# Kernel optimization log

Measured on AMD Instinct MI355X. Metric: run time of the kernel, lower is better.

## Reference

```python
import jax, jax.numpy as jnp
import numpy as np

K_HOPS = 2  # SGConv K = nlayers


def setup_inputs() -> dict:
    key = jax.random.key(0)
    k1, k2, k3 = jax.random.split(key, 3)
    N, E, F, C = 100000, 1600000, 128, 40
    x = jax.random.normal(k1, (N, F), dtype=jnp.float32)
    edge_index = jax.random.randint(k2, (2, E), 0, N, dtype=jnp.int64)
    W = jax.random.normal(k3, (C, F), dtype=jnp.float32) * (1.0 / np.sqrt(F))
    b = jnp.zeros((C,), dtype=jnp.float32)
    return {"x": x, "edge_index": edge_index, "W": W, "b": b}


def reference(x, edge_index, W, b):
    # SGConv: K hops of GCN-normalized propagation (with self-loops), then Linear.
    N = x.shape[0]
    loop = jnp.arange(N, dtype=edge_index.dtype)
    src = jnp.concatenate([edge_index[0], loop])  # message source
    dst = jnp.concatenate([edge_index[1], loop])  # aggregation target
    w = jnp.ones(src.shape[0], dtype=x.dtype)     # edge_weight=None -> 1, self-loop fill=1
    deg = jax.ops.segment_sum(w, dst, num_segments=N)  # in-degree incl. self-loop (>=1)
    dinv = jax.lax.rsqrt(deg)
    norm = dinv[src] * w * dinv[dst]              # D^{-1/2} A D^{-1/2}
    h = x
    for _ in range(K_HOPS):
        h = jax.ops.segment_sum(norm[:, None] * h[src], dst, num_segments=N)
    return h @ W.T + b
```

## Files before the change

kernel.cpp:

```cpp
#include <hip/hip_runtime.h>
#include <hip/hip_fp16.h>
#include <cstdint>

#define CDIM 40
#define FDIM 128
#define BIN_SHIFT 8
#define BIN_SZ (1 << BIN_SHIFT)
#define CHUNK 4096
#define STAGE_CAP 8192

typedef _Float16 f16x8 __attribute__((ext_vector_type(8)));
typedef float f32x4 __attribute__((ext_vector_type(4)));

static __device__ __forceinline__ long long load_idx(const void* p, int is64, long long i) {
    if (is64) return ((const long long*)p)[i];
    return (long long)((const int*)p)[i];
}

static __device__ __forceinline__ unsigned packh2(float a, float b) {
    __half2 h;
    h.x = __float2half(a);
    h.y = __float2half(b);
    return *(unsigned*)&h;
}

static __device__ __forceinline__ void addv4(float* acc, uint4 v) {
    const __half2* h = (const __half2*)&v;
    float2 f0 = __half22float2(h[0]);
    float2 f1 = __half22float2(h[1]);
    float2 f2 = __half22float2(h[2]);
    float2 f3 = __half22float2(h[3]);
    acc[0] += f0.x; acc[1] += f0.y; acc[2] += f1.x; acc[3] += f1.y;
    acc[4] += f2.x; acc[5] += f2.y; acc[6] += f3.x; acc[7] += f3.y;
}

static __device__ __forceinline__ f16x8 cvt8(float4 a, float4 b) {
    f16x8 r;
    r[0] = (_Float16)a.x; r[1] = (_Float16)a.y; r[2] = (_Float16)a.z; r[3] = (_Float16)a.w;
    r[4] = (_Float16)b.x; r[5] = (_Float16)b.y; r[6] = (_Float16)b.z; r[7] = (_Float16)b.w;
    return r;
}

__global__ void k_init(int* cursor, int nb, int capRec,
                       __half* gA0, __half* gB0, __half* gA1, __half* gB1, int N) {
    int i = blockIdx.x * blockDim.x + threadIdx.x;
    if (i < nb) cursor[i] = i * capRec;
    if (i < 40) {
        if (i < 16)      ((unsigned*)(gA0 + (size_t)N * 32))[i] = 0u;
        else if (i < 20) ((unsigned*)(gB0 + (size_t)N * 8))[i - 16] = 0u;
        else if (i < 36) ((unsigned*)(gA1 + (size_t)N * 32))[i - 20] = 0u;
        else             ((unsigned*)(gB1 + (size_t)N * 8))[i - 36] = 0u;
    }
}

__global__ __launch_bounds__(256) void kA3(const void* ei, long long E,
                                           int nb, int* __restrict__ cursor,
                                           unsigned* __restrict__ binned) {
    __shared__ unsigned lval[CHUNK];
    __shared__ unsigned short lbin[CHUNK];
    __shared__ int lcnt[512];
    __shared__ int lbase[512];
    __shared__ int lflag;
    int tid = threadIdx.x;
    if (tid == 0) lflag = 1;
    for (int i = tid; i < nb; i += 256) lcnt[i] = 0;
    __syncthreads();
    {
        const unsigned* w = (const unsigned*)ei;
        int nscan = (int)((2 * E < 4096) ? (2 * E) : 4096);
        for (int k = 1 + 2 * tid; k < nscan; k += 512)
            if (w[k] != 0u) lflag = 0;
    }
    __syncthreads();
    int is64 = lflag;
    long long base = (long long)blockIdx.x * CHUNK;
    int nk = (int)min((long long)CHUNK, E - base);
    for (int k = tid; k < nk; k += 256) {
        long long e = base + k;
        int s = (int)load_idx(ei, is64, e);
        int d = (int)load_idx(ei, is64, E + e);
        int bin = d >> BIN_SHIFT;
        lval[k] = (unsigned)s | ((unsigned)(d & (BIN_SZ - 1)) << 17);
        lbin[k] = (unsigned short)bin;
        atomicAdd(&lcnt[bin], 1);
    }
    __syncthreads();
    for (int i = tid; i < nb; i += 256) {
        int c = lcnt[i];
        lbase[i] = c ? atomicAdd(&cursor[i], c) : 0;
        lcnt[i] = 0;
    }
    __syncthreads();
    for (int k = tid; k < nk; k += 256) {
        int bin = lbin[k];
        int loc = atomicAdd(&lcnt[bin], 1);
        binned[lbase[bin] + loc] = lval[k];
    }
}

__global__ __launch_bounds__(256) void kBG(const unsigned* __restrict__ binned,
                                           const int* __restrict__ cursor,
                                           int capRec, int capC,
                                           int2* __restrict__ meta,
                                           int* __restrict__ cursorG,
                                           int* __restrict__ csr,
                                           const float* __restrict__ x,
                                           const float* __restrict__ W,
                                           __half* __restrict__ gA,
                                           __half* __restrict__ gB, int N) {
    __shared__ int lcnt[BIN_SZ];
    __shared__ int lsum[4];
    __shared__ int dh[64];
    __shared__ float dinvL[BIN_SZ];
    __shared__ int stage[STAGE_CAP];
    int b = blockIdx.x, tid = threadIdx.x;
    const int wid = tid >> 6;
    const int lane = tid & 63;
    int node0 = b << BIN_SHIFT;
    int nn = min(BIN_SZ, N - node0);
    int recBase = b * capRec;
    int csrBase = b * capC;
    int nedges = cursor[b] - recBase;

    lcnt[tid] = 0;
    if (tid < 64) dh[tid] = 0;
    __syncthreads();
    for (int t = tid; t < nedges; t += 256)
        atomicAdd(&lcnt[(binned[recBase + t] >> 17) & (BIN_SZ - 1)], 1);
    __syncthreads();
    int myc = lcnt[tid];
    int psz = (myc + 3) & ~3;
    int incl = psz;
#pragma unroll
    for (int off = 1; off < 64; off <<= 1) {
        int up = __shfl_up(incl, off, 64);
        if (lane >= off) incl += up;
    }
    if (lane == 63) lsum[wid] = incl;
    if (tid < nn) {
        dinvL[tid] = rsqrtf(1.0f + (float)myc);
        atomicAdd(&dh[min(myc, 63)], 1);
    } else {
        dinvL[tid] = 0.0f;
    }
    __syncthreads();
    int woff = 0;
#pragma unroll
    for (int w = 0; w < 4; ++w) woff += (w < wid) ? lsum[w] : 0;
    int ex = woff + incl - psz;
    int total = lsum[0] + lsum[1] + lsum[2] + lsum[3];
    if (wid == 0) {
        int dv = dh[lane];
        int di = dv;
#pragma unroll
        for (int off = 1; off < 64; off <<= 1) {
            int up = __shfl_up(di, off, 64);
            if (lane >= off) di += up;
        }
        dh[lane] = di - dv;
    }
    __syncthreads();
    if (tid < nn) {
        int pos = atomicAdd(&dh[min(myc, 63)], 1);
        int2 mi;
        mi.x = csrBase + ex;
        mi.y = (node0 + tid) | (myc << 17);
        meta[node0 + pos] = mi;
    }
    __syncthreads();
    lcnt[tid] = ex;
    __syncthreads();
    if (total <= STAGE_CAP) {
        for (int t = tid; t < total; t += 256) stage[t] = N;
        __syncthreads();
        for (int t = tid; t < nedges; t += 256) {
            unsigned v = binned[recBase + t];
            int src = (int)(v & 0x1FFFFu);
            int dl  = (int)((v >> 17) & (BIN_SZ - 1));
            int p = atomicAdd(&lcnt[dl], 1);
            stage[p] = src;
        }
        __syncthreads();
        const int4* sp = (const int4*)stage;
        int4* cp = (int4*)(csr + csrBase);
        for (int t = tid; t < (total >> 2); t += 256) cp[t] = sp[t];
    } else {
        if (tid < nn) cursorG[node0 + tid] = csrBase + ex;
        __syncthreads();
        for (int t = tid; t < nedges; t += 256) {
            unsigned v = binned[recBase + t];
            int src = (int)(v & 0x1FFFFu);
            int dl  = (int)((v >> 17) & (BIN_SZ - 1));
            int p = atomicAdd(&cursorG[node0 + dl], 1);
            csr[p] = src;
        }
        if (tid < nn)
            for (int k = myc; k < psz; ++k) csr[csrBase + ex + k] = N;
    }
    __syncthreads();

    const int m = lane & 15;
    const int quad = lane >> 4;
    f16x8 bfrag[3][4];
#pragma unroll
    for (int t = 0; t < 3; ++t) {
        int c = t * 16 + m;
#pragma unroll
        for (int q = 0; q < 4; ++q) {
            if (c < CDIM) {
                const float* wp = W + (size_t)c * FDIM + q * 32 + quad * 8;
                float4 w0 = *(const float4*)wp;
                float4 w1 = *(const float4*)(wp + 4);
                bfrag[t][q] = cvt8(w0, w1);
            } else {
                f16x8 z = {0, 0, 0, 0, 0, 0, 0, 0};
                bfrag[t][q] = z;
            }
        }
    }
#pragma unroll
    for (int i = 0; i < 4; ++i) {
        int lnode = wid * 64 + i * 16;
        int nodebase = node0 + lnode;
        if (nodebase >= N) break;
        const float* xp = x + (size_t)(nodebase + m) * FDIM + quad * 8;
        f16x8 afrag[4];
#pragma unroll
        for (int q = 0; q < 4; ++q) {
            float4 x0 = *(const float4*)(xp + q * 32);
            float4 x1 = *(const float4*)(xp + q * 32 + 4);
            afrag[q] = cvt8(x0, x1);
        }
        f32x4 acc0 = {0, 0, 0, 0}, acc1 = {0, 0, 0, 0}, acc2 = {0, 0, 0, 0};
#pragma unroll
        for (int q = 0; q < 4; ++q) {
            acc0 = __builtin_amdgcn_mfma_f32_16x16x32_f16(afrag[q], bfrag[0][q], acc0, 0, 0, 0);
            acc1 = __builtin_amdgcn_mfma_f32_16x16x32_f16(afrag[q], bfrag[1][q], acc1, 0, 0, 0);
            acc2 = __builtin_amdgcn_mfma_f32_16x16x32_f16(afrag[q], bfrag[2][q], acc2, 0, 0, 0);
        }
        float ds[4];
#pragma unroll
        for (int r = 0; r < 4; ++r) ds[r] = dinvL[lnode + quad * 4 + r];
#pragma unroll
        for (int r = 0; r < 4; ++r) {
            int node = nodebase + quad * 4 + r;
            gA[(size_t)node * 32 + m]      = __float2half(acc0[r] * ds[r]);
            gA[(size_t)node * 32 + 16 + m] = __float2half(acc1[r] * ds[r]);
            if (m < 8)
                gB[(size_t)node * 8 + m]   = __float2half(acc2[r] * ds[r]);
        }
    }
}

__global__ __launch_bounds__(256) void k_gather(const int2* __restrict__ meta,
                                                const int* __restrict__ csr,
                                                const __half* __restrict__ gA,
                                                const __half* __restrict__ gB,
                                                const float* __restrict__ b,
                                                __half* __restrict__ goA,
                                                __half* __restrict__ goB,
                                                float* __restrict__ outF,
                                                int N, int mode) {
    unsigned t = blockIdx.x * 256 + threadIdx.x;
    unsigned gidx = t / 5, c = t - gidx * 5;
    if (gidx >= (unsigned)N) return;
    int2 mi = meta[gidx];
    int j = mi.x;
    int node = mi.y & 0x1FFFF;
    int deg = mi.y >> 17;
    int end_pad = j + ((deg + 3) & ~3);
    const uint4* src;
    unsigned stride;
    if (c < 4) { src = (const uint4*)gA + c; stride = 4; }
    else       { src = (const uint4*)gB;     stride = 1; }
    float acc[8] = {0, 0, 0, 0, 0, 0, 0, 0};
    addv4(acc, src[(size_t)node * stride]);
    for (; j + 8 <= end_pad; j += 8) {
        int4 c0 = *(const int4*)&csr[j];
        int4 c1 = *(const int4*)&csr[j + 4];
        uint4 v0 = src[(size_t)c0.x * stride];
        uint4 v1 = src[(size_t)c0.y * stride];
        uint4 v2 = src[(size_t)c0.z * stride];
        uint4 v3 = src[(size_t)c0.w * stride];
        uint4 v4 = src[(size_t)c1.x * stride];
        uint4 v5 = src[(size_t)c1.y * stride];
        uint4 v6 = src[(size_t)c1.z * stride];
        uint4 v7 = src[(size_t)c1.w * stride];
        addv4(acc, v0); addv4(acc, v1); addv4(acc, v2); addv4(acc, v3);
        addv4(acc, v4); addv4(acc, v5); addv4(acc, v6); addv4(acc, v7);
    }
    if (j < end_pad) {
        int4 c0 = *(const int4*)&csr[j];
        uint4 v0 = src[(size_t)c0.x * stride];
        uint4 v1 = src[(size_t)c0.y * stride];
        uint4 v2 = src[(size_t)c0.z * stride];
        uint4 v3 = src[(size_t)c0.w * stride];
        addv4(acc, v0); addv4(acc, v1); addv4(acc, v2); addv4(acc, v3);
    }
    float d = rsqrtf(1.0f + (float)deg);
    if (mode == 0) {
        float s = d * d;
        uint4 o;
        o.x = packh2(acc[0] * s, acc[1] * s);
        o.y = packh2(acc[2] * s, acc[3] * s);
        o.z = packh2(acc[4] * s, acc[5] * s);
        o.w = packh2(acc[6] * s, acc[7] * s);
        if (c < 4) ((uint4*)goA)[(size_t)node * 4 + c] = o;
        else       ((uint4*)goB)[(size_t)node] = o;
    } else {
        float4 bv0 = ((const float4*)b)[2 * c];
        float4 bv1 = ((const float4*)b)[2 * c + 1];
        float4 o0, o1;
        o0.x = acc[0] * d + bv0.x;
        o0.y = acc[1] * d + bv0.y;
        o0.z = acc[2] * d + bv0.z;
        o0.w = acc[3] * d + bv0.w;
        o1.x = acc[4] * d + bv1.x;
        o1.y = acc[5] * d + bv1.y;
        o1.z = acc[6] * d + bv1.z;
        o1.w = acc[7] * d + bv1.w;
        ((float4*)outF)[(size_t)node * 10 + 2 * c]     = o0;
        ((float4*)outF)[(size_t)node * 10 + 2 * c + 1] = o1;
    }
}

static inline size_t align256(size_t v) { return (v + 255) & ~(size_t)255; }

extern "C" void kernel_launch(void* const* d_in, const int* in_sizes, int n_in,
                              void* d_out, int out_size, void* d_ws, size_t ws_size,
                              hipStream_t stream) {
    const float* x  = (const float*)d_in[0];
    const void*  ei = d_in[1];
    const float* W  = (const float*)d_in[2];
    const float* b  = (const float*)d_in[3];
    float* out = (float*)d_out;

    const int N = in_sizes[0] / FDIM;
    const long long E = (long long)in_sizes[1] / 2;

    const int nb     = (N + BIN_SZ - 1) >> BIN_SHIFT;
    const int nchunk = (int)((E + CHUNK - 1) / CHUNK);
    int capRec = (int)(E / nb) + 2048;
    if (capRec > STAGE_CAP) capRec = STAGE_CAP;
    int capC = (capRec + BIN_SZ * 3 + 1027) & ~3;

    char* wsb = (char*)d_ws;
    size_t off = 0;
    int*      cursor  = (int*)(wsb + off);      off = align256(off + (size_t)nb * 4);
    int*      cursorG = (int*)(wsb + off);      off = align256(off + (size_t)N * 4);
    int2*     meta    = (int2*)(wsb + off);     off = align256(off + (size_t)N * 8);
    __half*   gA0     = (__half*)(wsb + off);   off = align256(off + (size_t)(N + 1) * 32 * 2);
    __half*   gB0     = (__half*)(wsb + off);   off = align256(off + (size_t)(N + 1) * 8 * 2);
    __half*   gA1     = (__half*)(wsb + off);   off = align256(off + (size_t)(N + 1) * 32 * 2);
    __half*   gB1     = (__half*)(wsb + off);   off = align256(off + (size_t)(N + 1) * 8 * 2);
    unsigned* binned  = (unsigned*)(wsb + off); off = align256(off + (size_t)nb * capRec * 4);
    int*      csr     = (int*)(wsb + off);      off = align256(off + (size_t)nb * capC * 4);

    const int B = 256;
    const unsigned GT = 5u * (unsigned)N;
    const int nbGA = (int)((GT + B - 1) / B);

    k_init  <<<(nb + 255) / 256, 256, 0, stream>>>(cursor, nb, capRec, gA0, gB0, gA1, gB1, N);
    kA3     <<<nchunk, B, 0, stream>>>(ei, E, nb, cursor, binned);
    kBG     <<<nb, B, 0, stream>>>(binned, cursor, capRec, capC, meta, cursorG, csr,
                                   x, W, gA0, gB0, N);
    k_gather<<<nbGA, B, 0, stream>>>(meta, csr, gA0, gB0, b, gA1, gB1, nullptr, N, 0);
    k_gather<<<nbGA, B, 0, stream>>>(meta, csr, gA1, gB1, b, nullptr, nullptr, out, N, 1);
}
```

Before: 214.7 us.

## Replace two-level binned CSR build with global atomic degree count and scatter

Drops the edge binning pass and the per-bin LDS staging that built the CSR. The new scheme counts in-degrees with global atomics, scans per bin inside the projection kernel, then scatters source ids into CSR slots through global atomic cursors. This removes one full pass over the binned intermediate and its LDS footprint, but it reads edge_index twice and relies on contended, scattered global atomics, which can cost more than the old local sort. Edge order within each row also becomes nondeterministic.

```diff
diff --git a/kernel.cpp b/kernel.cpp
--- a/kernel.cpp
+++ b/kernel.cpp
@@ -6,8 +6,6 @@
 #define FDIM 128
 #define BIN_SHIFT 8
 #define BIN_SZ (1 << BIN_SHIFT)
-#define CHUNK 4096
-#define STAGE_CAP 8192
 
 typedef _Float16 f16x8 __attribute__((ext_vector_type(8)));
 typedef float f32x4 __attribute__((ext_vector_type(4)));
@@ -41,10 +39,11 @@
     return r;
 }
 
-__global__ void k_init(int* cursor, int nb, int capRec,
-                       __half* gA0, __half* gB0, __half* gA1, __half* gB1, int N) {
-    int i = blockIdx.x * blockDim.x + threadIdx.x;
-    if (i < nb) cursor[i] = i * capRec;
+__global__ __launch_bounds__(256) void k_init(int* deg, int N,
+                                              __half* gA0, __half* gB0,
+                                              __half* gA1, __half* gB1) {
+    int i = blockIdx.x * 256 + threadIdx.x;
+    if (i < N) deg[i] = 0;
     if (i < 40) {
         if (i < 16)      ((unsigned*)(gA0 + (size_t)N * 32))[i] = 0u;
         else if (i < 20) ((unsigned*)(gB0 + (size_t)N * 8))[i - 16] = 0u;
@@ -53,17 +52,11 @@
     }
 }
 
-__global__ __launch_bounds__(256) void kA3(const void* ei, long long E,
-                                           int nb, int* __restrict__ cursor,
-                                           unsigned* __restrict__ binned) {
-    __shared__ unsigned lval[CHUNK];
-    __shared__ unsigned short lbin[CHUNK];
-    __shared__ int lcnt[512];
-    __shared__ int lbase[512];
+__global__ __launch_bounds__(256) void k_count(const void* ei, long long E,
+                                               int* __restrict__ deg) {
     __shared__ int lflag;
     int tid = threadIdx.x;
     if (tid == 0) lflag = 1;
-    for (int i = tid; i < nb; i += 256) lcnt[i] = 0;
     __syncthreads();
     {
         const unsigned* w = (const unsigned*)ei;
@@ -73,62 +66,38 @@
     }
     __syncthreads();
     int is64 = lflag;
-    long long base = (long long)blockIdx.x * CHUNK;
-    int nk = (int)min((long long)CHUNK, E - base);
-    for (int k = tid; k < nk; k += 256) {
-        long long e = base + k;
-        int s = (int)load_idx(ei, is64, e);
-        int d = (int)load_idx(ei, is64, E + e);
-        int bin = d >> BIN_SHIFT;
-        lval[k] = (unsigned)s | ((unsigned)(d & (BIN_SZ - 1)) << 17);
-        lbin[k] = (unsigned short)bin;
-        atomicAdd(&lcnt[bin], 1);
-    }
-    __syncthreads();
-    for (int i = tid; i < nb; i += 256) {
-        int c = lcnt[i];
-        lbase[i] = c ? atomicAdd(&cursor[i], c) : 0;
-        lcnt[i] = 0;
-    }
-    __syncthreads();
-    for (int k = tid; k < nk; k += 256) {
-        int bin = lbin[k];
-        int loc = atomicAdd(&lcnt[bin], 1);
-        binned[lbase[bin] + loc] = lval[k];
-    }
-}
-
-__global__ __launch_bounds__(256) void kBG(const unsigned* __restrict__ binned,
-                                           const int* __restrict__ cursor,
-                                           int capRec, int capC,
-                                           int2* __restrict__ meta,
-                                           int* __restrict__ cursorG,
-                                           int* __restrict__ csr,
-                                           const float* __restrict__ x,
-                                           const float* __restrict__ W,
-                                           __half* __restrict__ gA,
-                                           __half* __restrict__ gB, int N) {
-    __shared__ int lcnt[BIN_SZ];
+    long long base = (long long)blockIdx.x * 1024;
+#pragma unroll
+    for (int p = 0; p < 4; ++p) {
+        long long e = base + p * 256 + tid;
+        if (e < E) {
+            int d = (int)load_idx(ei, is64, E + e);
+            atomicAdd(&deg[d], 1);
+        }
+    }
+}
+
+__global__ __launch_bounds__(256) void k_scanG(const int* __restrict__ deg,
+                                               int capC,
+                                               int2* __restrict__ meta,
+                                               int* __restrict__ cursor,
+                                               int* __restrict__ csr,
+                                               const float* __restrict__ x,
+                                               const float* __restrict__ W,
+                                               __half* __restrict__ gA,
+                                               __half* __restrict__ gB, int N) {
     __shared__ int lsum[4];
     __shared__ int dh[64];
     __shared__ float dinvL[BIN_SZ];
-    __shared__ int stage[STAGE_CAP];
     int b = blockIdx.x, tid = threadIdx.x;
     const int wid = tid >> 6;
     const int lane = tid & 63;
     int node0 = b << BIN_SHIFT;
     int nn = min(BIN_SZ, N - node0);
-    int recBase = b * capRec;
     int csrBase = b * capC;
-    int nedges = cursor[b] - recBase;
-
-    lcnt[tid] = 0;
+
     if (tid < 64) dh[tid] = 0;
-    __syncthreads();
-    for (int t = tid; t < nedges; t += 256)
-        atomicAdd(&lcnt[(binned[recBase + t] >> 17) & (BIN_SZ - 1)], 1);
-    __syncthreads();
-    int myc = lcnt[tid];
+    int myc = (tid < nn) ? deg[node0 + tid] : 0;
     int psz = (myc + 3) & ~3;
     int incl = psz;
 #pragma unroll
@@ -137,18 +106,14 @@
         if (lane >= off) incl += up;
     }
     if (lane == 63) lsum[wid] = incl;
-    if (tid < nn) {
-        dinvL[tid] = rsqrtf(1.0f + (float)myc);
-        atomicAdd(&dh[min(myc, 63)], 1);
-    } else {
-        dinvL[tid] = 0.0f;
-    }
-    __syncthreads();
+    dinvL[tid] = (tid < nn) ? rsqrtf(1.0f + (float)myc) : 0.0f;
+    __syncthreads();
+    if (tid < nn) atomicAdd(&dh[min(myc, 63)], 1);
     int woff = 0;
 #pragma unroll
     for (int w = 0; w < 4; ++w) woff += (w < wid) ? lsum[w] : 0;
     int ex = woff + incl - psz;
-    int total = lsum[0] + lsum[1] + lsum[2] + lsum[3];
+    __syncthreads();
     if (wid == 0) {
         int dv = dh[lane];
         int di = dv;
@@ -166,38 +131,9 @@
         mi.x = csrBase + ex;
         mi.y = (node0 + tid) | (myc << 17);
         meta[node0 + pos] = mi;
-    }
-    __syncthreads();
-    lcnt[tid] = ex;
-    __syncthreads();
-    if (total <= STAGE_CAP) {
-        for (int t = tid; t < total; t += 256) stage[t] = N;
-        __syncthreads();
-        for (int t = tid; t < nedges; t += 256) {
-            unsigned v = binned[recBase + t];
-            int src = (int)(v & 0x1FFFFu);
-            int dl  = (int)((v >> 17) & (BIN_SZ - 1));
-            int p = atomicAdd(&lcnt[dl], 1);
-            stage[p] = src;
-        }
-        __syncthreads();
-        const int4* sp = (const int4*)stage;
-        int4* cp = (int4*)(csr + csrBase);
-        for (int t = tid; t < (total >> 2); t += 256) cp[t] = sp[t];
-    } else {
-        if (tid < nn) cursorG[node0 + tid] = csrBase + ex;
-        __syncthreads();
-        for (int t = tid; t < nedges; t += 256) {
-            unsigned v = binned[recBase + t];
-            int src = (int)(v & 0x1FFFFu);
-            int dl  = (int)((v >> 17) & (BIN_SZ - 1));
-            int p = atomicAdd(&cursorG[node0 + dl], 1);
-            csr[p] = src;
-        }
-        if (tid < nn)
-            for (int k = myc; k < psz; ++k) csr[csrBase + ex + k] = N;
-    }
-    __syncthreads();
+        cursor[node0 + tid] = csrBase + ex;
+        for (int k = myc; k < psz; ++k) csr[csrBase + ex + k] = N;
+    }
 
     const int m = lane & 15;
     const int quad = lane >> 4;
@@ -218,6 +154,7 @@
             }
         }
     }
+    __syncthreads();
 #pragma unroll
     for (int i = 0; i < 4; ++i) {
         int lnode = wid * 64 + i * 16;
@@ -248,6 +185,34 @@
             gA[(size_t)node * 32 + 16 + m] = __float2half(acc1[r] * ds[r]);
             if (m < 8)
                 gB[(size_t)node * 8 + m]   = __float2half(acc2[r] * ds[r]);
+        }
+    }
+}
+
+__global__ __launch_bounds__(256) void k_scatter(const void* ei, long long E,
+                                                 int* __restrict__ cursor,
+                                                 int* __restrict__ csr) {
+    __shared__ int lflag;
+    int tid = threadIdx.x;
+    if (tid == 0) lflag = 1;
+    __syncthreads();
+    {
+        const unsigned* w = (const unsigned*)ei;
+        int nscan = (int)((2 * E < 4096) ? (2 * E) : 4096);
+        for (int k = 1 + 2 * tid; k < nscan; k += 512)
+            if (w[k] != 0u) lflag = 0;
+    }
+    __syncthreads();
+    int is64 = lflag;
+    long long base = (long long)blockIdx.x * 1024;
+#pragma unroll
+    for (int p = 0; p < 4; ++p) {
+        long long e = base + p * 256 + tid;
+        if (e < E) {
+            int s = (int)load_idx(ei, is64, e);
+            int d = (int)load_idx(ei, is64, E + e);
+            int pos = atomicAdd(&cursor[d], 1);
+            csr[pos] = s;
         }
     }
 }
@@ -338,32 +303,31 @@
     const int N = in_sizes[0] / FDIM;
     const long long E = (long long)in_sizes[1] / 2;
 
-    const int nb     = (N + BIN_SZ - 1) >> BIN_SHIFT;
-    const int nchunk = (int)((E + CHUNK - 1) / CHUNK);
+    const int nb = (N + BIN_SZ - 1) >> BIN_SHIFT;
     int capRec = (int)(E / nb) + 2048;
-    if (capRec > STAGE_CAP) capRec = STAGE_CAP;
     int capC = (capRec + BIN_SZ * 3 + 1027) & ~3;
 
     char* wsb = (char*)d_ws;
     size_t off = 0;
-    int*      cursor  = (int*)(wsb + off);      off = align256(off + (size_t)nb * 4);
-    int*      cursorG = (int*)(wsb + off);      off = align256(off + (size_t)N * 4);
+    int*      cursor  = (int*)(wsb + off);      off = align256(off + (size_t)N * 4);
+    int*      deg     = (int*)(wsb + off);      off = align256(off + (size_t)N * 4);
     int2*     meta    = (int2*)(wsb + off);     off = align256(off + (size_t)N * 8);
     __half*   gA0     = (__half*)(wsb + off);   off = align256(off + (size_t)(N + 1) * 32 * 2);
     __half*   gB0     = (__half*)(wsb + off);   off = align256(off + (size_t)(N + 1) * 8 * 2);
     __half*   gA1     = (__half*)(wsb + off);   off = align256(off + (size_t)(N + 1) * 32 * 2);
     __half*   gB1     = (__half*)(wsb + off);   off = align256(off + (size_t)(N + 1) * 8 * 2);
-    unsigned* binned  = (unsigned*)(wsb + off); off = align256(off + (size_t)nb * capRec * 4);
     int*      csr     = (int*)(wsb + off);      off = align256(off + (size_t)nb * capC * 4);
 
     const int B = 256;
+    const int nbN  = (N + 255) / 256;
+    const int nbE  = (int)((E + 1023) / 1024);
     const unsigned GT = 5u * (unsigned)N;
     const int nbGA = (int)((GT + B - 1) / B);
 
-    k_init  <<<(nb + 255) / 256, 256, 0, stream>>>(cursor, nb, capRec, gA0, gB0, gA1, gB1, N);
-    kA3     <<<nchunk, B, 0, stream>>>(ei, E, nb, cursor, binned);
-    kBG     <<<nb, B, 0, stream>>>(binned, cursor, capRec, capC, meta, cursorG, csr,
-                                   x, W, gA0, gB0, N);
-    k_gather<<<nbGA, B, 0, stream>>>(meta, csr, gA0, gB0, b, gA1, gB1, nullptr, N, 0);
-    k_gather<<<nbGA, B, 0, stream>>>(meta, csr, gA1, gB1, b, nullptr, nullptr, out, N, 1);
-}
+    k_init   <<<nbN, B, 0, stream>>>(deg, N, gA0, gB0, gA1, gB1);
+    k_count  <<<nbE, B, 0, stream>>>(ei, E, deg);
+    k_scanG  <<<nb, B, 0, stream>>>(deg, capC, meta, cursor, csr, x, W, gA0, gB0, N);
+    k_scatter<<<nbE, B, 0, stream>>>(ei, E, cursor, csr);
+    k_gather <<<nbGA, B, 0, stream>>>(meta, csr, gA0, gB0, b, gA1, gB1, nullptr, N, 0);
+    k_gather <<<nbGA, B, 0, stream>>>(meta, csr, gA1, gB1, b, nullptr, nullptr, out, N, 1);
+}
```

Result: slower. 380.7 us (+77.3%).

## Replace atomic-cursor edge binning with count, scan, scatter passes

Applied to the files above, without the earlier changes.

Edge binning by destination moves from a single kernel that stages a chunk in shared memory and reserves per-bin space with global atomics to three kernels. A per-chunk histogram pass writes a chunk×bin count matrix, a per-bin scan turns it into deterministic write offsets, and a scatter pass writes records straight to global memory. The chunk size is halved so more blocks run. This drops the global atomic contention and the shared staging, at the cost of reading the edge list twice and adding two extra launches plus a strided count matrix.

```diff
diff --git a/kernel.cpp b/kernel.cpp
--- a/kernel.cpp
+++ b/kernel.cpp
@@ -6,7 +6,7 @@
 #define FDIM 128
 #define BIN_SHIFT 8
 #define BIN_SZ (1 << BIN_SHIFT)
-#define CHUNK 4096
+#define CHUNK 2048
 #define STAGE_CAP 8192
 
 typedef _Float16 f16x8 __attribute__((ext_vector_type(8)));
@@ -41,29 +41,83 @@
     return r;
 }
 
-__global__ void k_init(int* cursor, int nb, int capRec,
-                       __half* gA0, __half* gB0, __half* gA1, __half* gB1, int N) {
-    int i = blockIdx.x * blockDim.x + threadIdx.x;
-    if (i < nb) cursor[i] = i * capRec;
-    if (i < 40) {
-        if (i < 16)      ((unsigned*)(gA0 + (size_t)N * 32))[i] = 0u;
-        else if (i < 20) ((unsigned*)(gB0 + (size_t)N * 8))[i - 16] = 0u;
-        else if (i < 36) ((unsigned*)(gA1 + (size_t)N * 32))[i - 20] = 0u;
-        else             ((unsigned*)(gB1 + (size_t)N * 8))[i - 36] = 0u;
-    }
-}
-
-__global__ __launch_bounds__(256) void kA3(const void* ei, long long E,
-                                           int nb, int* __restrict__ cursor,
-                                           unsigned* __restrict__ binned) {
-    __shared__ unsigned lval[CHUNK];
-    __shared__ unsigned short lbin[CHUNK];
+__global__ __launch_bounds__(256) void k_cnt(const void* ei, long long E,
+                                             int nb, int* __restrict__ cnt,
+                                             __half* gA0, __half* gB0,
+                                             __half* gA1, __half* gB1, int N) {
+    __shared__ int lcnt[512];
+    __shared__ int lflag;
+    int tid = threadIdx.x;
+    if (blockIdx.x == 0 && tid < 40) {
+        if (tid < 16)      ((unsigned*)(gA0 + (size_t)N * 32))[tid] = 0u;
+        else if (tid < 20) ((unsigned*)(gB0 + (size_t)N * 8))[tid - 16] = 0u;
+        else if (tid < 36) ((unsigned*)(gA1 + (size_t)N * 32))[tid - 20] = 0u;
+        else               ((unsigned*)(gB1 + (size_t)N * 8))[tid - 36] = 0u;
+    }
+    if (tid == 0) lflag = 1;
+    for (int i = tid; i < nb; i += 256) lcnt[i] = 0;
+    __syncthreads();
+    {
+        const unsigned* w = (const unsigned*)ei;
+        int nscan = (int)((2 * E < 4096) ? (2 * E) : 4096);
+        for (int k = 1 + 2 * tid; k < nscan; k += 512)
+            if (w[k] != 0u) lflag = 0;
+    }
+    __syncthreads();
+    int is64 = lflag;
+    long long base = (long long)blockIdx.x * CHUNK;
+    int nk = (int)min((long long)CHUNK, E - base);
+    for (int k = tid; k < nk; k += 256) {
+        int d = (int)load_idx(ei, is64, E + base + k);
+        atomicAdd(&lcnt[d >> BIN_SHIFT], 1);
+    }
+    __syncthreads();
+    for (int i = tid; i < nb; i += 256)
+        cnt[(size_t)blockIdx.x * nb + i] = lcnt[i];
+}
+
+__global__ __launch_bounds__(256) void k_scan(int* __restrict__ cnt,
+                                              int* __restrict__ binTot,
+                                              int nchunk, int nb, int capRec) {
+    __shared__ int lsum[4];
+    int b = blockIdx.x, tid = threadIdx.x;
+    const int wid = tid >> 6;
+    const int lane = tid & 63;
+    int running = b * capRec;
+    for (int c0 = 0; c0 < nchunk; c0 += 256) {
+        int c = c0 + tid;
+        int v = (c < nchunk) ? cnt[(size_t)c * nb + b] : 0;
+        int incl = v;
+#pragma unroll
+        for (int off = 1; off < 64; off <<= 1) {
+            int up = __shfl_up(incl, off, 64);
+            if (lane >= off) incl += up;
+        }
+        if (lane == 63) lsum[wid] = incl;
+        __syncthreads();
+        int woff = 0;
+#pragma unroll
+        for (int w = 0; w < 4; ++w) woff += (w < wid) ? lsum[w] : 0;
+        int total = lsum[0] + lsum[1] + lsum[2] + lsum[3];
+        if (c < nchunk) cnt[(size_t)c * nb + b] = running + woff + incl - v;
+        running += total;
+        __syncthreads();
+    }
+    if (tid == 0) binTot[b] = running - b * capRec;
+}
+
+__global__ __launch_bounds__(256) void k_scat(const void* ei, long long E,
+                                              int nb, const int* __restrict__ cnt,
+                                              unsigned* __restrict__ binned) {
     __shared__ int lcnt[512];
     __shared__ int lbase[512];
     __shared__ int lflag;
     int tid = threadIdx.x;
     if (tid == 0) lflag = 1;
-    for (int i = tid; i < nb; i += 256) lcnt[i] = 0;
+    for (int i = tid; i < nb; i += 256) {
+        lcnt[i] = 0;
+        lbase[i] = cnt[(size_t)blockIdx.x * nb + i];
+    }
     __syncthreads();
     {
         const unsigned* w = (const unsigned*)ei;
@@ -80,26 +134,13 @@
         int s = (int)load_idx(ei, is64, e);
         int d = (int)load_idx(ei, is64, E + e);
         int bin = d >> BIN_SHIFT;
-        lval[k] = (unsigned)s | ((unsigned)(d & (BIN_SZ - 1)) << 17);
-        lbin[k] = (unsigned short)bin;
-        atomicAdd(&lcnt[bin], 1);
-    }
-    __syncthreads();
-    for (int i = tid; i < nb; i += 256) {
-        int c = lcnt[i];
-        lbase[i] = c ? atomicAdd(&cursor[i], c) : 0;
-        lcnt[i] = 0;
-    }
-    __syncthreads();
-    for (int k = tid; k < nk; k += 256) {
-        int bin = lbin[k];
         int loc = atomicAdd(&lcnt[bin], 1);
-        binned[lbase[bin] + loc] = lval[k];
+        binned[lbase[bin] + loc] = (unsigned)s | ((unsigned)(d & (BIN_SZ - 1)) << 17);
     }
 }
 
 __global__ __launch_bounds__(256) void kBG(const unsigned* __restrict__ binned,
-                                           const int* __restrict__ cursor,
+                                           const int* __restrict__ binTot,
                                            int capRec, int capC,
                                            int2* __restrict__ meta,
                                            int* __restrict__ cursorG,
@@ -120,7 +161,7 @@
     int nn = min(BIN_SZ, N - node0);
     int recBase = b * capRec;
     int csrBase = b * capC;
-    int nedges = cursor[b] - recBase;
+    int nedges = binTot[b];
 
     lcnt[tid] = 0;
     if (tid < 64) dh[tid] = 0;
@@ -346,7 +387,8 @@
 
     char* wsb = (char*)d_ws;
     size_t off = 0;
-    int*      cursor  = (int*)(wsb + off);      off = align256(off + (size_t)nb * 4);
+    int*      cnt     = (int*)(wsb + off);      off = align256(off + (size_t)nchunk * nb * 4);
+    int*      binTot  = (int*)(wsb + off);      off = align256(off + (size_t)nb * 4);
     int*      cursorG = (int*)(wsb + off);      off = align256(off + (size_t)N * 4);
     int2*     meta    = (int2*)(wsb + off);     off = align256(off + (size_t)N * 8);
     __half*   gA0     = (__half*)(wsb + off);   off = align256(off + (size_t)(N + 1) * 32 * 2);
@@ -360,9 +402,10 @@
     const unsigned GT = 5u * (unsigned)N;
     const int nbGA = (int)((GT + B - 1) / B);
 
-    k_init  <<<(nb + 255) / 256, 256, 0, stream>>>(cursor, nb, capRec, gA0, gB0, gA1, gB1, N);
-    kA3     <<<nchunk, B, 0, stream>>>(ei, E, nb, cursor, binned);
-    kBG     <<<nb, B, 0, stream>>>(binned, cursor, capRec, capC, meta, cursorG, csr,
+    k_cnt   <<<nchunk, B, 0, stream>>>(ei, E, nb, cnt, gA0, gB0, gA1, gB1, N);
+    k_scan  <<<nb, B, 0, stream>>>(cnt, binTot, nchunk, nb, capRec);
+    k_scat  <<<nchunk, B, 0, stream>>>(ei, E, nb, cnt, binned);
+    kBG     <<<nb, B, 0, stream>>>(binned, binTot, capRec, capC, meta, cursorG, csr,
                                    x, W, gA0, gB0, N);
     k_gather<<<nbGA, B, 0, stream>>>(meta, csr, gA0, gB0, b, gA1, gB1, nullptr, N, 0);
     k_gather<<<nbGA, B, 0, stream>>>(meta, csr, gA1, gB1, b, nullptr, nullptr, out, N, 1);
```

Result: slower. 222.9 us (+3.8%).

## Split fused CSR build and projection GEMM into separate kernels

Applied to the files above, without the earlier changes.

The fused bin-processing kernel is split into k_build, which writes the CSR and per-node dinv to global memory, and k_gemm, which runs the x·Wᵀ MFMA projection over 64-node blocks with far more blocks. The LDS staging buffer and the global-atomic fallback are removed, so CSR entries are now scattered straight to global memory. The init kernel becomes a memset, and the kA3 chunk size is halved. This is meant to raise occupancy and parallelism for the GEMM and cut LDS use, at the cost of an extra launch, a dinv round-trip through memory, and uncoalesced CSR writes.

```diff
diff --git a/kernel.cpp b/kernel.cpp
--- a/kernel.cpp
+++ b/kernel.cpp
@@ -6,8 +6,7 @@
 #define FDIM 128
 #define BIN_SHIFT 8
 #define BIN_SZ (1 << BIN_SHIFT)
-#define CHUNK 4096
-#define STAGE_CAP 8192
+#define CHUNK 2048
 
 typedef _Float16 f16x8 __attribute__((ext_vector_type(8)));
 typedef float f32x4 __attribute__((ext_vector_type(4)));
@@ -41,20 +40,9 @@
     return r;
 }
 
-__global__ void k_init(int* cursor, int nb, int capRec,
-                       __half* gA0, __half* gB0, __half* gA1, __half* gB1, int N) {
-    int i = blockIdx.x * blockDim.x + threadIdx.x;
-    if (i < nb) cursor[i] = i * capRec;
-    if (i < 40) {
-        if (i < 16)      ((unsigned*)(gA0 + (size_t)N * 32))[i] = 0u;
-        else if (i < 20) ((unsigned*)(gB0 + (size_t)N * 8))[i - 16] = 0u;
-        else if (i < 36) ((unsigned*)(gA1 + (size_t)N * 32))[i - 20] = 0u;
-        else             ((unsigned*)(gB1 + (size_t)N * 8))[i - 36] = 0u;
-    }
-}
-
 __global__ __launch_bounds__(256) void kA3(const void* ei, long long E,
-                                           int nb, int* __restrict__ cursor,
+                                           int nb, int capRec,
+                                           int* __restrict__ cursor,
                                            unsigned* __restrict__ binned) {
     __shared__ unsigned lval[CHUNK];
     __shared__ unsigned short lbin[CHUNK];
@@ -94,34 +82,34 @@
     for (int k = tid; k < nk; k += 256) {
         int bin = lbin[k];
         int loc = atomicAdd(&lcnt[bin], 1);
-        binned[lbase[bin] + loc] = lval[k];
-    }
-}
-
-__global__ __launch_bounds__(256) void kBG(const unsigned* __restrict__ binned,
-                                           const int* __restrict__ cursor,
-                                           int capRec, int capC,
-                                           int2* __restrict__ meta,
-                                           int* __restrict__ cursorG,
-                                           int* __restrict__ csr,
-                                           const float* __restrict__ x,
-                                           const float* __restrict__ W,
-                                           __half* __restrict__ gA,
-                                           __half* __restrict__ gB, int N) {
+        binned[(size_t)bin * capRec + lbase[bin] + loc] = lval[k];
+    }
+}
+
+__global__ __launch_bounds__(256) void k_build(const unsigned* __restrict__ binned,
+                                               const int* __restrict__ cursor,
+                                               int capRec, int capC,
+                                               int2* __restrict__ meta,
+                                               float* __restrict__ dinv,
+                                               int* __restrict__ csr,
+                                               __half* __restrict__ gA1,
+                                               __half* __restrict__ gB1, int N) {
     __shared__ int lcnt[BIN_SZ];
     __shared__ int lsum[4];
     __shared__ int dh[64];
-    __shared__ float dinvL[BIN_SZ];
-    __shared__ int stage[STAGE_CAP];
     int b = blockIdx.x, tid = threadIdx.x;
     const int wid = tid >> 6;
     const int lane = tid & 63;
     int node0 = b << BIN_SHIFT;
     int nn = min(BIN_SZ, N - node0);
-    int recBase = b * capRec;
+    size_t recBase = (size_t)b * capRec;
     int csrBase = b * capC;
-    int nedges = cursor[b] - recBase;
-
+    int nedges = cursor[b];
+
+    if (b == 0 && tid < 20) {
+        if (tid < 16) ((unsigned*)(gA1 + (size_t)N * 32))[tid] = 0u;
+        else          ((unsigned*)(gB1 + (size_t)N * 8))[tid - 16] = 0u;
+    }
     lcnt[tid] = 0;
     if (tid < 64) dh[tid] = 0;
     __syncthreads();
@@ -138,17 +126,14 @@
     }
     if (lane == 63) lsum[wid] = incl;
     if (tid < nn) {
-        dinvL[tid] = rsqrtf(1.0f + (float)myc);
+        dinv[node0 + tid] = rsqrtf(1.0f + (float)myc);
         atomicAdd(&dh[min(myc, 63)], 1);
-    } else {
-        dinvL[tid] = 0.0f;
     }
     __syncthreads();
     int woff = 0;
 #pragma unroll
     for (int w = 0; w < 4; ++w) woff += (w < wid) ? lsum[w] : 0;
     int ex = woff + incl - psz;
-    int total = lsum[0] + lsum[1] + lsum[2] + lsum[3];
     if (wid == 0) {
         int dv = dh[lane];
         int di = dv;
@@ -166,41 +151,33 @@
         mi.x = csrBase + ex;
         mi.y = (node0 + tid) | (myc << 17);
         meta[node0 + pos] = mi;
-    }
-    __syncthreads();
-    lcnt[tid] = ex;
-    __syncthreads();
-    if (total <= STAGE_CAP) {
-        for (int t = tid; t < total; t += 256) stage[t] = N;
-        __syncthreads();
-        for (int t = tid; t < nedges; t += 256) {
-            unsigned v = binned[recBase + t];
-            int src = (int)(v & 0x1FFFFu);
-            int dl  = (int)((v >> 17) & (BIN_SZ - 1));
-            int p = atomicAdd(&lcnt[dl], 1);
-            stage[p] = src;
-        }
-        __syncthreads();
-        const int4* sp = (const int4*)stage;
-        int4* cp = (int4*)(csr + csrBase);
-        for (int t = tid; t < (total >> 2); t += 256) cp[t] = sp[t];
-    } else {
-        if (tid < nn) cursorG[node0 + tid] = csrBase + ex;
-        __syncthreads();
-        for (int t = tid; t < nedges; t += 256) {
-            unsigned v = binned[recBase + t];
-            int src = (int)(v & 0x1FFFFu);
-            int dl  = (int)((v >> 17) & (BIN_SZ - 1));
-            int p = atomicAdd(&cursorG[node0 + dl], 1);
-            csr[p] = src;
-        }
-        if (tid < nn)
-            for (int k = myc; k < psz; ++k) csr[csrBase + ex + k] = N;
-    }
-    __syncthreads();
-
-    const int m = lane & 15;
-    const int quad = lane >> 4;
+        for (int k = myc; k < psz; ++k) csr[csrBase + ex + k] = N;
+    }
+    __syncthreads();
+    lcnt[tid] = csrBase + ex;
+    __syncthreads();
+    for (int t = tid; t < nedges; t += 256) {
+        unsigned v = binned[recBase + t];
+        int src = (int)(v & 0x1FFFFu);
+        int dl  = (int)((v >> 17) & (BIN_SZ - 1));
+        int p = atomicAdd(&lcnt[dl], 1);
+        csr[p] = src;
+    }
+}
+
+__global__ __launch_bounds__(256) void k_gemm(const float* __restrict__ x,
+                                              const float* __restrict__ W,
+                                              const float* __restrict__ dinv,
+                                              __half* __restrict__ gA,
+                                              __half* __restrict__ gB, int N) {
+    if (blockIdx.x == 0 && threadIdx.x < 20) {
+        if (threadIdx.x < 16) ((unsigned*)(gA + (size_t)N * 32))[threadIdx.x] = 0u;
+        else                  ((unsigned*)(gB + (size_t)N * 8))[threadIdx.x - 16] = 0u;
+    }
+    int wid = threadIdx.x >> 6;
+    int lane = threadIdx.x & 63;
+    int m = lane & 15;
+    int quad = lane >> 4;
     f16x8 bfrag[3][4];
 #pragma unroll
     for (int t = 0; t < 3; ++t) {
@@ -218,37 +195,32 @@
             }
         }
     }
-#pragma unroll
-    for (int i = 0; i < 4; ++i) {
-        int lnode = wid * 64 + i * 16;
-        int nodebase = node0 + lnode;
-        if (nodebase >= N) break;
-        const float* xp = x + (size_t)(nodebase + m) * FDIM + quad * 8;
-        f16x8 afrag[4];
-#pragma unroll
-        for (int q = 0; q < 4; ++q) {
-            float4 x0 = *(const float4*)(xp + q * 32);
-            float4 x1 = *(const float4*)(xp + q * 32 + 4);
-            afrag[q] = cvt8(x0, x1);
-        }
-        f32x4 acc0 = {0, 0, 0, 0}, acc1 = {0, 0, 0, 0}, acc2 = {0, 0, 0, 0};
-#pragma unroll
-        for (int q = 0; q < 4; ++q) {
-            acc0 = __builtin_amdgcn_mfma_f32_16x16x32_f16(afrag[q], bfrag[0][q], acc0, 0, 0, 0);
-            acc1 = __builtin_amdgcn_mfma_f32_16x16x32_f16(afrag[q], bfrag[1][q], acc1, 0, 0, 0);
-            acc2 = __builtin_amdgcn_mfma_f32_16x16x32_f16(afrag[q], bfrag[2][q], acc2, 0, 0, 0);
-        }
-        float ds[4];
-#pragma unroll
-        for (int r = 0; r < 4; ++r) ds[r] = dinvL[lnode + quad * 4 + r];
-#pragma unroll
-        for (int r = 0; r < 4; ++r) {
-            int node = nodebase + quad * 4 + r;
-            gA[(size_t)node * 32 + m]      = __float2half(acc0[r] * ds[r]);
-            gA[(size_t)node * 32 + 16 + m] = __float2half(acc1[r] * ds[r]);
-            if (m < 8)
-                gB[(size_t)node * 8 + m]   = __float2half(acc2[r] * ds[r]);
-        }
+    int nodebase = blockIdx.x * 64 + wid * 16;
+    if (nodebase >= N) return;
+    const float* xp = x + (size_t)(nodebase + m) * FDIM + quad * 8;
+    f16x8 afrag[4];
+#pragma unroll
+    for (int q = 0; q < 4; ++q) {
+        float4 x0 = *(const float4*)(xp + q * 32);
+        float4 x1 = *(const float4*)(xp + q * 32 + 4);
+        afrag[q] = cvt8(x0, x1);
+    }
+    f32x4 acc0 = {0, 0, 0, 0}, acc1 = {0, 0, 0, 0}, acc2 = {0, 0, 0, 0};
+#pragma unroll
+    for (int q = 0; q < 4; ++q) {
+        acc0 = __builtin_amdgcn_mfma_f32_16x16x32_f16(afrag[q], bfrag[0][q], acc0, 0, 0, 0);
+        acc1 = __builtin_amdgcn_mfma_f32_16x16x32_f16(afrag[q], bfrag[1][q], acc1, 0, 0, 0);
+        acc2 = __builtin_amdgcn_mfma_f32_16x16x32_f16(afrag[q], bfrag[2][q], acc2, 0, 0, 0);
+    }
+    float4 dvv = *(const float4*)&dinv[nodebase + quad * 4];
+    float ds[4] = {dvv.x, dvv.y, dvv.z, dvv.w};
+#pragma unroll
+    for (int r = 0; r < 4; ++r) {
+        int node = nodebase + quad * 4 + r;
+        gA[(size_t)node * 32 + m]      = __float2half(acc0[r] * ds[r]);
+        gA[(size_t)node * 32 + 16 + m] = __float2half(acc1[r] * ds[r]);
+        if (m < 8)
+            gB[(size_t)node * 8 + m]   = __float2half(acc2[r] * ds[r]);
     }
 }
 
@@ -341,13 +313,12 @@
     const int nb     = (N + BIN_SZ - 1) >> BIN_SHIFT;
     const int nchunk = (int)((E + CHUNK - 1) / CHUNK);
     int capRec = (int)(E / nb) + 2048;
-    if (capRec > STAGE_CAP) capRec = STAGE_CAP;
     int capC = (capRec + BIN_SZ * 3 + 1027) & ~3;
 
     char* wsb = (char*)d_ws;
     size_t off = 0;
     int*      cursor  = (int*)(wsb + off);      off = align256(off + (size_t)nb * 4);
-    int*      cursorG = (int*)(wsb + off);      off = align256(off + (size_t)N * 4);
+    float*    dinv    = (float*)(wsb + off);    off = align256(off + (size_t)N * 4);
     int2*     meta    = (int2*)(wsb + off);     off = align256(off + (size_t)N * 8);
     __half*   gA0     = (__half*)(wsb + off);   off = align256(off + (size_t)(N + 1) * 32 * 2);
     __half*   gB0     = (__half*)(wsb + off);   off = align256(off + (size_t)(N + 1) * 8 * 2);
@@ -357,13 +328,15 @@
     int*      csr     = (int*)(wsb + off);      off = align256(off + (size_t)nb * capC * 4);
 
     const int B = 256;
+    const int nbGE = (N + 63) / 64;
     const unsigned GT = 5u * (unsigned)N;
     const int nbGA = (int)((GT + B - 1) / B);
 
-    k_init  <<<(nb + 255) / 256, 256, 0, stream>>>(cursor, nb, capRec, gA0, gB0, gA1, gB1, N);
-    kA3     <<<nchunk, B, 0, stream>>>(ei, E, nb, cursor, binned);
-    kBG     <<<nb, B, 0, stream>>>(binned, cursor, capRec, capC, meta, cursorG, csr,
-                                   x, W, gA0, gB0, N);
+    hipMemsetAsync(cursor, 0, (size_t)nb * 4, stream);
+    kA3     <<<nchunk, B, 0, stream>>>(ei, E, nb, capRec, cursor, binned);
+    k_build <<<nb, B, 0, stream>>>(binned, cursor, capRec, capC, meta, dinv, csr,
+                                   gA1, gB1, N);
+    k_gemm  <<<nbGE, B, 0, stream>>>(x, W, dinv, gA0, gB0, N);
     k_gather<<<nbGA, B, 0, stream>>>(meta, csr, gA0, gB0, b, gA1, gB1, nullptr, N, 0);
     k_gather<<<nbGA, B, 0, stream>>>(meta, csr, gA1, gB1, b, nullptr, nullptr, out, N, 1);
 }
```

Result: slower. 233.9 us (+8.9%).
